# Performance work log

Hardware: AMD Instinct MI355X
Metric: run time of the kernel (lower is better)

The kernel has to match this reference:

```python
import jax, jax.numpy as jnp
import numpy as np

INNER = 256   # inner_channel
NODES = 64    # nodes_num (prototypes)
EM_NUM = 3
DIAG_C = 128  # hardcoded diag_channel in FullyConnectGCLayer


def setup_inputs() -> dict:
    key = jax.random.key(0)
    ks = jax.random.split(key, 16)
    b, c, w, h = 4, 1024, 64, 64
    f32 = jnp.float32
    d = {}
    d["x"] = jax.random.normal(ks[0], (b, c, w, h), f32)
    # Conv2d weights re-initialized to N(0, 0.001) in Intra_graph.__init__
    d["W_in"] = 0.001 * jax.random.normal(ks[1], (INNER, c), f32)
    d["b_in"] = jnp.zeros((INNER,), f32)
    d["multi_proto"] = 0.001 * jax.random.normal(ks[2], (1, INNER, NODES), f32)
    d["pi0"] = jnp.ones((1, NODES), f32) / NODES
    # Conv1d layers keep default kaiming-uniform-ish init
    lim = 1.0 / np.sqrt(INNER)
    d["W_adj"] = jax.random.uniform(ks[3], (DIAG_C, INNER), f32, -lim, lim)
    d["b_adj"] = jax.random.uniform(ks[4], (DIAG_C,), f32, -lim, lim)
    d["W_diag"] = jax.random.uniform(ks[5], (DIAG_C, INNER), f32, -lim, lim)
    d["b_diag"] = jax.random.uniform(ks[6], (DIAG_C,), f32, -lim, lim)
    d["gcn_weight"] = 0.01 * jax.random.normal(ks[7], (INNER, INNER), f32)
    d["W_out"] = 0.001 * jax.random.normal(ks[8], (c, INNER), f32)
    d["b_out"] = jnp.zeros((c,), f32)
    d["gamma"] = jnp.ones((c,), f32)
    d["beta"] = jnp.zeros((c,), f32)
    d["W_out2"] = 0.001 * jax.random.normal(ks[9], (c, INNER), f32)
    d["b_out2"] = jnp.zeros((c,), f32)
    d["gamma2"] = jnp.ones((c,), f32)
    d["beta2"] = jnp.zeros((c,), f32)
    d["flag"] = 0
    return d


def _bn(y, g, bt):
    # BatchNorm2d in training mode: batch stats over (N,H,W), biased var, eps=1e-5
    m = jnp.mean(y, (0, 2, 3), keepdims=True)
    v = jnp.var(y, (0, 2, 3), keepdims=True)
    return (y - m) * jax.lax.rsqrt(v + 1e-5) * g[None, :, None, None] + bt[None, :, None, None]


def _forward(x, W_in, b_in, multi_proto, pi0, W_adj, b_adj, W_diag, b_diag,
             gcn_weight, W_out, b_out, gamma, beta, W_out2, b_out2, gamma2, beta2):
    b, c, w, h = x.shape
    wh = w * h
    x1 = (jnp.einsum('oi,bihw->bohw', W_in, x) + b_in[None, :, None, None]).reshape(b, INNER, wh)
    # ---- EM soft-clustering loop (runs under no_grad in torch) ----
    x1s = jax.lax.stop_gradient(x1)
    mu = jnp.broadcast_to(multi_proto, (b, INNER, NODES))
    pi = jnp.broadcast_to(pi0[None, :, :], (b, 1, NODES))
    for _ in range(EM_NUM):
        lik = jnp.einsum('bcm,bcn->bmn', x1s, mu)              # [b, wh, n]
        lik = jnp.exp(lik - jnp.max(lik, 2, keepdims=True))
        post = lik * pi
        post = post / (1e-18 + jnp.sum(post, 2, keepdims=True))
        prob = post / (1e-18 + jnp.sum(post, 1, keepdims=True))
        mu = jnp.einsum('bcm,bmn->bcn', x1s, prob)
        pi = jnp.sum(post, 1, keepdims=True) / wh
    post = jax.lax.stop_gradient(post)
    prob = jax.lax.stop_gradient(prob)
    # ---- aggregate to prototypes (grad flows through x1 only) ----
    x2 = jnp.einsum('bcm,bmn->bcn', x1, prob)                   # [b, inner, n]
    # ---- branch 2: scatter back, conv, bn ----
    x4 = jnp.einsum('bcn,bmn->bcm', x2, post).reshape(b, INNER, w, h)
    x4 = _bn(jnp.einsum('oi,bihw->bohw', W_out2, x4) + b_out2[None, :, None, None], gamma2, beta2)
    output2 = jax.nn.relu(jax.nn.relu(x4) + x)
    # ---- FullyConnectGCLayer on x2 ----
    xd = jnp.einsum('oi,bin->bon', W_diag, x2) + b_diag[None, :, None]
    dvec = jax.nn.sigmoid(jnp.mean(xd, 2))                      # [b, 128]
    xa = jnp.einsum('oi,bin->bon', W_adj, x2) + b_adj[None, :, None]  # [b, 128, n]
    # sigmoid(diag(d)) has 0.5 off-diagonal, sigmoid(d) on diagonal:
    # xa^T S xa = 0.5 * (1^T xa)^T (1^T xa) + xa^T diag(sig(d)-0.5) xa
    u = jnp.sum(xa, 1)                                          # [b, n]
    A = 0.5 * u[:, :, None] * u[:, None, :] + jnp.einsum('bcn,bc,bcm->bnm', xa, dvec - 0.5, xa)
    A = jax.nn.relu(A) + jnp.eye(NODES, dtype=x.dtype)[None]
    deg = jax.lax.stop_gradient(jnp.sum(A, 1) ** -0.5)          # no_grad degree, [b, n]
    A = deg[:, :, None] * A * deg[:, None, :]
    gout = jnp.einsum('oi,bin->bon', gcn_weight, jnp.einsum('bcn,bnm->bcm', x2, A))
    x2g = jax.nn.relu(gout) + x2                                # res_connect
    # ---- branch 1: scatter back, conv, bn ----
    x3 = jnp.einsum('bcn,bmn->bcm', x2g, post).reshape(b, INNER, w, h)
    x3 = _bn(jnp.einsum('oi,bihw->bohw', W_out, x3) + b_out[None, :, None, None], gamma, beta)
    output = jax.nn.relu(jax.nn.relu(x3) + x)
    return output, output2


def reference(x, W_in, b_in, multi_proto, pi0, W_adj, b_adj, W_diag, b_diag,
              gcn_weight, W_out, b_out, gamma, beta, W_out2, b_out2, gamma2, beta2, flag):
    # flag only gates a buffer EMA update (no effect on forward outputs)
    return _forward(x, W_in, b_in, multi_proto, pi0, W_adj, b_adj, W_diag, b_diag,
                    gcn_weight, W_out, b_out, gamma, beta, W_out2, b_out2, gamma2, beta2)
```

## Files before the change

### kernel.cpp

```cpp
#include <hip/hip_runtime.h>
#include <math.h>


typedef unsigned short u16;
typedef short s16x8 __attribute__((ext_vector_type(8)));
typedef float f32x4 __attribute__((ext_vector_type(4)));

constexpr int BB  = 4;
constexpr int CH  = 1024;
constexpr int IN  = 256;
constexpr int ND  = 64;
constexpr int WH  = 4096;
constexpr int DCN = 128;
constexpr size_t TOT = (size_t)BB * CH * WH;

__device__ inline u16 f2bf(float f) {
  unsigned u = __float_as_uint(f);
  return (u16)((u + 0x7fffu + ((u >> 16) & 1u)) >> 16);
}
__device__ inline s16x8 ld8(const u16* p) { return *(const s16x8*)p; }
#define MFMA16(a, b, c) __builtin_amdgcn_mfma_f32_16x16x32_bf16(a, b, c, 0, 0, 0)

__global__ void k_init(const float* __restrict__ Win, const float* __restrict__ mp,
                       const float* __restrict__ pi0, u16* __restrict__ Winb,
                       u16* __restrict__ mu_t, float* __restrict__ piw,
                       float* __restrict__ sp) {
  int idx = blockIdx.x * 256 + threadIdx.x;
  if (idx < IN * CH) { Winb[idx] = f2bf(Win[idx]); return; }
  int j = idx - IN * CH;
  if (j < BB * ND * IN) {
    int bb = j >> 14, n = (j >> 8) & 63, c = j & 255;
    mu_t[((size_t)(bb * ND + n)) * IN + c] = f2bf(mp[c * ND + n]);
    return;
  }
  j -= BB * ND * IN;
  if (j < BB * ND) { piw[j] = pi0[j & 63]; return; }
  j -= BB * ND;
  if (j < 3 * BB * ND) sp[j] = 0.f;
}

__global__ __launch_bounds__(512) void k_x1(
    const float* __restrict__ x, const u16* __restrict__ Winb,
    const float* __restrict__ bin, u16* __restrict__ x1, u16* __restrict__ x1t) {
  __shared__ u16 lt[64][40];
  const int t = threadIdx.x, w = t >> 6, lr = t & 15, lg = (t >> 4) & 3;
  const int wc = w & 3, wm = w >> 2;
  const int m0 = blockIdx.x * 64, b = blockIdx.y;
  const int si = t >> 4, sm = (t & 15) * 4;
  const float* xb = x + (size_t)b * CH * WH + m0 + sm;
  f32x4 acc[4][2];
#pragma unroll
  for (int i = 0; i < 4; ++i)
#pragma unroll
    for (int j = 0; j < 2; ++j) acc[i][j] = (f32x4){0.f, 0.f, 0.f, 0.f};
  const u16* wp = Winb + (size_t)(wc * 64 + lr) * CH + lg * 8;

  float4 nxt = *(const float4*)&xb[(size_t)si * WH];
  for (int k0 = 0; k0 < CH; k0 += 32) {
    float4 cur = nxt;
    __syncthreads();
    lt[sm + 0][si] = f2bf(cur.x); lt[sm + 1][si] = f2bf(cur.y);
    lt[sm + 2][si] = f2bf(cur.z); lt[sm + 3][si] = f2bf(cur.w);
    if (k0 + 32 < CH) nxt = *(const float4*)&xb[(size_t)(k0 + 32 + si) * WH];
    __syncthreads();
    s16x8 af[4], bf[2];
#pragma unroll
    for (int i = 0; i < 4; ++i) af[i] = ld8(wp + (size_t)i * 16 * CH + k0);
#pragma unroll
    for (int j = 0; j < 2; ++j) bf[j] = *(const s16x8*)&lt[wm * 32 + j * 16 + lr][lg * 8];
#pragma unroll
    for (int i = 0; i < 4; ++i)
#pragma unroll
      for (int j = 0; j < 2; ++j) acc[i][j] = MFMA16(af[i], bf[j], acc[i][j]);
  }
#pragma unroll
  for (int i = 0; i < 4; ++i) {
    const int cb = wc * 64 + i * 16 + lg * 4;
    const float4 bi = *(const float4*)&bin[cb];
    const float bia[4] = {bi.x, bi.y, bi.z, bi.w};
#pragma unroll
    for (int j = 0; j < 2; ++j) {
      const int m = m0 + wm * 32 + j * 16 + lr;
      float v[4];
#pragma unroll
      for (int r = 0; r < 4; ++r) v[r] = acc[i][j][r] + bia[r];
      ushort4 o;
      o.x = f2bf(v[0]); o.y = f2bf(v[1]); o.z = f2bf(v[2]); o.w = f2bf(v[3]);
      *(ushort4*)&x1t[((size_t)b * WH + m) * IN + cb] = o;
#pragma unroll
      for (int r = 0; r < 4; ++r)
        x1[((size_t)b * IN + cb + r) * WH + m] = f2bf(v[r]);
    }
  }
}

__global__ __launch_bounds__(256) void k_em(
    const u16* __restrict__ x1, const u16* __restrict__ x1t,
    const u16* __restrict__ mu_t, const float* __restrict__ piw,
    float* __restrict__ sp, u16* __restrict__ pmn,
    float* __restrict__ mup, float* __restrict__ gp, int doLast) {
  __shared__ u16 ptl[64][264];
  const int t = threadIdx.x, w = t >> 6, lr = t & 15, lg = (t >> 4) & 3;
  const int mch = blockIdx.x, b = blockIdx.y;
  const int mbase = mch * 256;
  {
    f32x4 acc[4][4];
#pragma unroll
    for (int i = 0; i < 4; ++i)
#pragma unroll
      for (int f = 0; f < 4; ++f) acc[i][f] = (f32x4){0.f, 0.f, 0.f, 0.f};
    const u16* ap = x1t + ((size_t)b * WH + mbase + w * 64 + lr) * IN + lg * 8;
    const u16* bp = mu_t + ((size_t)b * ND + lr) * IN + lg * 8;
#pragma unroll
    for (int k0 = 0; k0 < IN; k0 += 32) {
      s16x8 bf[4];
#pragma unroll
      for (int f = 0; f < 4; ++f) bf[f] = ld8(bp + f * 16 * IN + k0);
#pragma unroll
      for (int i = 0; i < 4; ++i) {
        s16x8 av = ld8(ap + (size_t)i * 16 * IN + k0);
#pragma unroll
        for (int f = 0; f < 4; ++f) acc[i][f] = MFMA16(av, bf[f], acc[i][f]);
      }
    }
    float pi_[4], spart[4] = {0.f, 0.f, 0.f, 0.f};
#pragma unroll
    for (int f = 0; f < 4; ++f) pi_[f] = piw[b * ND + f * 16 + lr];
#pragma unroll
    for (int i = 0; i < 4; ++i)
#pragma unroll
      for (int r = 0; r < 4; ++r) {
        float v0 = acc[i][0][r], v1 = acc[i][1][r], v2 = acc[i][2][r], v3 = acc[i][3][r];
        float mx = fmaxf(fmaxf(v0, v1), fmaxf(v2, v3));
        mx = fmaxf(mx, __shfl_xor(mx, 1)); mx = fmaxf(mx, __shfl_xor(mx, 2));
        mx = fmaxf(mx, __shfl_xor(mx, 4)); mx = fmaxf(mx, __shfl_xor(mx, 8));
        float e0 = __expf(v0 - mx) * pi_[0], e1 = __expf(v1 - mx) * pi_[1];
        float e2 = __expf(v2 - mx) * pi_[2], e3 = __expf(v3 - mx) * pi_[3];
        float s = e0 + e1 + e2 + e3;
        s += __shfl_xor(s, 1); s += __shfl_xor(s, 2);
        s += __shfl_xor(s, 4); s += __shfl_xor(s, 8);
        const float inv = 1.f / (1e-18f + s);
        e0 *= inv; e1 *= inv; e2 *= inv; e3 *= inv;
        const int mloc = w * 64 + i * 16 + lg * 4 + r;
        u16 q0 = f2bf(e0), q1 = f2bf(e1), q2 = f2bf(e2), q3 = f2bf(e3);
        ptl[0 + lr][mloc]  = q0; ptl[16 + lr][mloc] = q1;
        ptl[32 + lr][mloc] = q2; ptl[48 + lr][mloc] = q3;
        if (doLast) {
          const size_t gbase = ((size_t)b * WH + mbase + mloc) * ND + lr;
          pmn[gbase + 0]  = q0; pmn[gbase + 16] = q1;
          pmn[gbase + 32] = q2; pmn[gbase + 48] = q3;
        }
        spart[0] += e0; spart[1] += e1; spart[2] += e2; spart[3] += e3;
      }
#pragma unroll
    for (int f = 0; f < 4; ++f) {
      spart[f] += __shfl_xor(spart[f], 16);
      spart[f] += __shfl_xor(spart[f], 32);
    }
    if (((t >> 4) & 3) == 0) {
#pragma unroll
      for (int f = 0; f < 4; ++f)
        atomicAdd(&sp[b * ND + f * 16 + lr], spart[f]);
    }
  }
  __syncthreads();
  {
    f32x4 acc[4][4];
#pragma unroll
    for (int i = 0; i < 4; ++i)
#pragma unroll
      for (int j = 0; j < 4; ++j) acc[i][j] = (f32x4){0.f, 0.f, 0.f, 0.f};
    const u16* ap = x1 + ((size_t)b * IN + w * 64 + lr) * WH + mbase + lg * 8;
#pragma unroll
    for (int ks = 0; ks < 8; ++ks) {
      s16x8 af[4], bf[4];
#pragma unroll
      for (int i = 0; i < 4; ++i) af[i] = ld8(ap + (size_t)i * 16 * WH + ks * 32);
#pragma unroll
      for (int j = 0; j < 4; ++j)
        bf[j] = *(const s16x8*)&ptl[j * 16 + lr][ks * 32 + lg * 8];
#pragma unroll
      for (int i = 0; i < 4; ++i)
#pragma unroll
        for (int j = 0; j < 4; ++j) acc[i][j] = MFMA16(af[i], bf[j], acc[i][j]);
    }
    float* mo = mup + ((size_t)mch * BB + b) * (IN * ND);
#pragma unroll
    for (int i = 0; i < 4; ++i)
#pragma unroll
      for (int j = 0; j < 4; ++j)
#pragma unroll
        for (int r = 0; r < 4; ++r) {
          const int c = w * 64 + i * 16 + lg * 4 + r, n = j * 16 + lr;
          mo[c * ND + n] = acc[i][j][r];
        }
  }
  if (doLast) {
    f32x4 acc[4];
#pragma unroll
    for (int j = 0; j < 4; ++j) acc[j] = (f32x4){0.f, 0.f, 0.f, 0.f};
#pragma unroll
    for (int ks = 0; ks < 8; ++ks) {
      s16x8 av = *(const s16x8*)&ptl[w * 16 + lr][ks * 32 + lg * 8];
#pragma unroll
      for (int j = 0; j < 4; ++j) {
        s16x8 bq = *(const s16x8*)&ptl[j * 16 + lr][ks * 32 + lg * 8];
        acc[j] = MFMA16(av, bq, acc[j]);
      }
    }
    float* go = gp + ((size_t)mch * BB + b) * (ND * ND);
#pragma unroll
    for (int j = 0; j < 4; ++j)
#pragma unroll
      for (int r = 0; r < 4; ++r) {
        const int n1 = w * 16 + lg * 4 + r, n2 = j * 16 + lr;
        go[n1 * ND + n2] = acc[j][r];
      }
  }
}

__global__ void k_mu_red(const float* __restrict__ mup, const float* __restrict__ spb,
                         float* __restrict__ piw, float* __restrict__ mu,
                         u16* __restrict__ mu_t, const float* __restrict__ gp,
                         float* __restrict__ G, int doG) {
  const int idx = blockIdx.x * 256 + threadIdx.x;
  const int bb = idx >> 14, c = (idx >> 6) & 255, n = idx & 63;
  float s = 0.f;
#pragma unroll
  for (int ch = 0; ch < 16; ++ch)
    s += mup[((size_t)ch * BB + bb) * (IN * ND) + (idx & 16383)];
  const float v = s / (1e-18f + spb[bb * ND + n]);
  mu[idx] = v;
  mu_t[((size_t)(bb * ND + n)) * IN + c] = f2bf(v);
  if (idx < BB * ND) piw[idx] = spb[idx] * (1.f / (float)WH);
  if (doG && idx < BB * ND * ND) {
    float g = 0.f;
#pragma unroll
    for (int ch = 0; ch < 16; ++ch) g += gp[(size_t)ch * (BB * ND * ND) + idx];
    G[idx] = g;
  }
}

__device__ void zg_body(const float* __restrict__ W, const float* __restrict__ v,
                        float* __restrict__ z, u16* __restrict__ zb,
                        int o0, int bb, int t, char* smem) {
  float (*As)[68] = (float(*)[68])smem;
  float (*Bs)[64] = (float(*)[64])(smem + 4352);
  const int tx = t & 15, ty = t >> 4;
  const int aoo = t >> 2, akq = (t & 3) * 4;
  const int bkk = t >> 4, bnq = (t & 15) * 4;
  float acc[4][4] = {};
  for (int k0 = 0; k0 < IN; k0 += 16) {
    {
      float4 w4 = *(const float4*)&W[(size_t)(o0 + aoo) * IN + k0 + akq];
      As[akq + 0][aoo] = w4.x; As[akq + 1][aoo] = w4.y;
      As[akq + 2][aoo] = w4.z; As[akq + 3][aoo] = w4.w;
    }
    *(float4*)&Bs[bkk][bnq] = *(const float4*)&v[((size_t)bb * IN + k0 + bkk) * ND + bnq];
    __syncthreads();
#pragma unroll
    for (int kk = 0; kk < 16; ++kk) {
      float4 a4 = *(const float4*)&As[kk][ty * 4];
      float4 b4 = *(const float4*)&Bs[kk][tx * 4];
      float ar[4] = {a4.x, a4.y, a4.z, a4.w}, br[4] = {b4.x, b4.y, b4.z, b4.w};
#pragma unroll
      for (int i = 0; i < 4; ++i)
#pragma unroll
        for (int j = 0; j < 4; ++j) acc[i][j] += ar[i] * br[j];
    }
    __syncthreads();
  }
#pragma unroll
  for (int i = 0; i < 4; ++i) {
    float4 r = make_float4(acc[i][0], acc[i][1], acc[i][2], acc[i][3]);
    const size_t off = ((size_t)bb * CH + o0 + ty * 4 + i) * ND + tx * 4;
    *(float4*)&z[off] = r;
    ushort4 h;
    h.x = f2bf(r.x); h.y = f2bf(r.y); h.z = f2bf(r.z); h.w = f2bf(r.w);
    *(ushort4*)&zb[off] = h;
  }
}

__global__ __launch_bounds__(256) void k_gcAz2(
    const float* __restrict__ mu, const float* __restrict__ gw,
    const float* __restrict__ Wa, const float* __restrict__ ba,
    const float* __restrict__ Wd, const float* __restrict__ bd,
    float* __restrict__ qbuf, float* __restrict__ xabuf, float* __restrict__ dv,
    const float* __restrict__ Wo2, float* __restrict__ z2, u16* __restrict__ zb2) {
  __shared__ __align__(16) char smem[66560];
  const int t = threadIdx.x, bid = blockIdx.x;
  if (bid < 28) {
    const int blk = bid % 7, b = bid / 7;
    float* sx2 = (float*)smem;
    float* srm = (float*)(smem + 65536);
    if (blk < 6) {
      const float* src = mu + (size_t)b * IN * ND;
#pragma unroll
      for (int q4 = 0; q4 < 16; ++q4)
        *(float4*)&sx2[q4 * 1024 + t * 4] = *(const float4*)&src[q4 * 1024 + t * 4];
      __syncthreads();
      const int rg = t >> 4, cg2 = t & 15;
      const float* W = (blk < 4) ? gw + (size_t)(blk * 64 + rg * 4) * IN
                                 : Wa + (size_t)((blk - 4) * 64 + rg * 4) * IN;
      float acc[4][4] = {};
      for (int i4 = 0; i4 < 64; ++i4) {
        float4 xv[4];
#pragma unroll
        for (int e = 0; e < 4; ++e)
          xv[e] = *(const float4*)&sx2[(i4 * 4 + e) * 64 + cg2 * 4];
#pragma unroll
        for (int rr = 0; rr < 4; ++rr) {
          const float4 w4 = *(const float4*)&W[(size_t)rr * IN + i4 * 4];
          acc[rr][0] += w4.x * xv[0].x + w4.y * xv[1].x + w4.z * xv[2].x + w4.w * xv[3].x;
          acc[rr][1] += w4.x * xv[0].y + w4.y * xv[1].y + w4.z * xv[2].y + w4.w * xv[3].y;
          acc[rr][2] += w4.x * xv[0].z + w4.y * xv[1].z + w4.z * xv[2].z + w4.w * xv[3].z;
          acc[rr][3] += w4.x * xv[0].w + w4.y * xv[1].w + w4.z * xv[2].w + w4.w * xv[3].w;
        }
      }
      if (blk < 4) {
        float* dst = qbuf + (size_t)b * IN * ND + (size_t)(blk * 64 + rg * 4) * ND + cg2 * 4;
#pragma unroll
        for (int rr = 0; rr < 4; ++rr)
          *(float4*)&dst[(size_t)rr * ND] =
              make_float4(acc[rr][0], acc[rr][1], acc[rr][2], acc[rr][3]);
      } else {
        const int xr = (blk - 4) * 64 + rg * 4;
        float* dst = xabuf + (size_t)b * DCN * ND + (size_t)xr * ND + cg2 * 4;
#pragma unroll
        for (int rr = 0; rr < 4; ++rr) {
          const float bv = ba[xr + rr];
          *(float4*)&dst[(size_t)rr * ND] =
              make_float4(acc[rr][0] + bv, acc[rr][1] + bv, acc[rr][2] + bv, acc[rr][3] + bv);
        }
      }
    } else {
      {
        const float* row = mu + (size_t)b * IN * ND + (size_t)t * ND;
        float s = 0.f;
#pragma unroll
        for (int n4 = 0; n4 < 16; ++n4) {
          float4 v = *(const float4*)&row[n4 * 4];
          s += v.x + v.y + v.z + v.w;
        }
        srm[t] = s * (1.f / ND);
      }
      __syncthreads();
      if (t < DCN) {
        float av = 0.f;
#pragma unroll
        for (int i4 = 0; i4 < 64; ++i4) {
          float4 w4 = *(const float4*)&Wd[(size_t)t * IN + i4 * 4];
          float4 r4 = *(const float4*)&srm[i4 * 4];
          av += w4.x * r4.x + w4.y * r4.y + w4.z * r4.z + w4.w * r4.w;
        }
        av += bd[t];
        dv[b * DCN + t] = 1.f / (1.f + __expf(-av)) - 0.5f;
      }
    }
  } else if (bid >= 32 && bid < 96) {
    const int zid = bid - 32;
    zg_body(Wo2, mu, z2, zb2, (zid & 15) * 64, zid >> 4, t, smem);
  }
}

__global__ __launch_bounds__(256) void k_gcBC(
    const float* __restrict__ xabuf, const float* __restrict__ dv,
    const float* __restrict__ qbuf, const float* __restrict__ mu,
    float* __restrict__ x2g) {
  __shared__ float sxa[DCN * ND];
  __shared__ float sA[ND * 65];
  __shared__ float sq[64 * 68];
  __shared__ float sdv[DCN];
  __shared__ float su[ND];
  __shared__ float sdeg[ND];
  const int t = threadIdx.x, qtr = blockIdx.x, b = blockIdx.y;
  {
    const float* src = xabuf + (size_t)b * DCN * ND;
#pragma unroll
    for (int q4 = 0; q4 < 8; ++q4)
      *(float4*)&sxa[q4 * 1024 + t * 4] = *(const float4*)&src[q4 * 1024 + t * 4];
    if (t < DCN) sdv[t] = dv[b * DCN + t];
    const int r = t >> 2, seg = (t & 3) * 16;
    const float* qs = qbuf + (size_t)b * IN * ND + (size_t)(qtr * 64 + r) * ND + seg;
#pragma unroll
    for (int f = 0; f < 4; ++f) {
      float4 v = *(const float4*)&qs[f * 4];
      sq[r * 68 + seg + f * 4 + 0] = v.x; sq[r * 68 + seg + f * 4 + 1] = v.y;
      sq[r * 68 + seg + f * 4 + 2] = v.z; sq[r * 68 + seg + f * 4 + 3] = v.w;
    }
  }
  __syncthreads();
  if (t < ND) {
    float s = 0.f;
    for (int dc = 0; dc < DCN; ++dc) s += sxa[dc * ND + t];
    su[t] = s;
  }
  __syncthreads();
  {
    const int n1g = t >> 4, n2g = t & 15;
    float acc[4][4] = {};
    for (int dc = 0; dc < DCN; ++dc) {
      const float dvv = sdv[dc];
      float4 v1 = *(const float4*)&sxa[dc * ND + n1g * 4];
      const float4 v2 = *(const float4*)&sxa[dc * ND + n2g * 4];
      v1.x *= dvv; v1.y *= dvv; v1.z *= dvv; v1.w *= dvv;
      acc[0][0] += v1.x * v2.x; acc[0][1] += v1.x * v2.y;
      acc[0][2] += v1.x * v2.z; acc[0][3] += v1.x * v2.w;
      acc[1][0] += v1.y * v2.x; acc[1][1] += v1.y * v2.y;
      acc[1][2] += v1.y * v2.z; acc[1][3] += v1.y * v2.w;
      acc[2][0] += v1.z * v2.x; acc[2][1] += v1.z * v2.y;
      acc[2][2] += v1.z * v2.z; acc[2][3] += v1.z * v2.w;
      acc[3][0] += v1.w * v2.x; acc[3][1] += v1.w * v2.y;
      acc[3][2] += v1.w * v2.z; acc[3][3] += v1.w * v2.w;
    }
#pragma unroll
    for (int i = 0; i < 4; ++i) {
      const int n1 = n1g * 4 + i;
      const float u1 = su[n1];
#pragma unroll
      for (int j = 0; j < 4; ++j) {
        const int n2 = n2g * 4 + j;
        const float v = acc[i][j] + 0.5f * u1 * su[n2];
        sA[n1 * 65 + n2] = fmaxf(v, 0.f) + (n1 == n2 ? 1.f : 0.f);
      }
    }
  }
  __syncthreads();
  if (t < ND) {
    float s = 0.f;
    for (int m = 0; m < ND; ++m) s += sA[m * 65 + t];
    sdeg[t] = rsqrtf(s);
  }
  __syncthreads();
  {
    const int n1g = t >> 4, n2g = t & 15;
#pragma unroll
    for (int i = 0; i < 4; ++i) {
      const int n1 = n1g * 4 + i;
      const float dr = sdeg[n1];
#pragma unroll
      for (int e = 0; e < 4; ++e)
        sA[n1 * 65 + n2g * 4 + e] *= dr * sdeg[n2g * 4 + e];
    }
  }
  __syncthreads();
  {
    const int rg = t >> 4, cg2 = t & 15;
    float acc[4][4] = {};
    for (int k = 0; k < ND; ++k) {
      const float4 a4 = *(const float4*)&sA[k * 65 + cg2 * 4];
      float qv[4];
#pragma unroll
      for (int rr = 0; rr < 4; ++rr) qv[rr] = sq[(rg * 4 + rr) * 68 + k];
#pragma unroll
      for (int rr = 0; rr < 4; ++rr) {
        acc[rr][0] += qv[rr] * a4.x; acc[rr][1] += qv[rr] * a4.y;
        acc[rr][2] += qv[rr] * a4.z; acc[rr][3] += qv[rr] * a4.w;
      }
    }
#pragma unroll
    for (int rr = 0; rr < 4; ++rr) {
      const size_t off = (size_t)b * IN * ND + (size_t)(qtr * 64 + rg * 4 + rr) * ND + cg2 * 4;
      const float4 xv = *(const float4*)&mu[off];
      float4 o;
      o.x = fmaxf(acc[rr][0], 0.f) + xv.x; o.y = fmaxf(acc[rr][1], 0.f) + xv.y;
      o.z = fmaxf(acc[rr][2], 0.f) + xv.z; o.w = fmaxf(acc[rr][3], 0.f) + xv.w;
      *(float4*)&x2g[off] = o;
    }
  }
}

__global__ __launch_bounds__(256) void k_zg(
    const float* __restrict__ W, const float* __restrict__ v,
    float* __restrict__ z, u16* __restrict__ zb) {
  __shared__ __align__(16) char smem[8448];
  zg_body(W, v, z, zb, blockIdx.x * 64, blockIdx.y, threadIdx.x, smem);
}

__global__ __launch_bounds__(256) void k_stats(
    const float* __restrict__ z1, const float* __restrict__ z2,
    const float* __restrict__ sp, const float* __restrict__ G,
    const float* __restrict__ gam, const float* __restrict__ bet,
    const float* __restrict__ gam2, const float* __restrict__ bet2,
    float* __restrict__ abc) {
  const int t = threadIdx.x;
  const int o = blockIdx.x * 4 + (t >> 6), lane = t & 63;
#pragma unroll
  for (int br = 0; br < 2; ++br) {
    const float* z = br ? z2 : z1;
    float macc = 0.f, eacc = 0.f;
    for (int bb = 0; bb < BB; ++bb) {
      const float zv = z[((size_t)bb * CH + o) * ND + lane];
      float s1 = zv * sp[bb * ND + lane];
      const float* Gb = G + (size_t)bb * ND * ND;
      float gz = 0.f;
      for (int k = 0; k < ND; ++k) {
        const float zk = __shfl(zv, k);
        gz += Gb[k * ND + lane] * zk;
      }
      float q = zv * gz;
#pragma unroll
      for (int off = 32; off; off >>= 1) {
        s1 += __shfl_xor(s1, off);
        q  += __shfl_xor(q, off);
      }
      macc += s1; eacc += q;
    }
    const float inv = 1.f / (float)((size_t)BB * WH);
    const float mean = macc * inv;
    const float var  = eacc * inv - mean * mean;
    const float a = (br ? gam2[o] : gam[o]) * rsqrtf(var + 1e-5f);
    const float c = (br ? bet2[o] : bet[o]) - mean * a;
    if (lane == 0) { abc[br * 2 * CH + o] = a; abc[br * 2 * CH + CH + o] = c; }
  }
}

__global__ __launch_bounds__(256) void k_epi(
    const u16* __restrict__ zb1, const u16* __restrict__ zb2,
    const u16* __restrict__ post, const float* __restrict__ abc,
    const float* __restrict__ x, float* __restrict__ out1, float* __restrict__ out2) {
  const int t = threadIdx.x, w = t >> 6, lr = t & 15, lg = (t >> 4) & 3;
  const int m0 = blockIdx.x * 256 + w * 64, o0 = blockIdx.y * 64, bb = blockIdx.z;
  f32x4 acc1[4][4], acc2[4][4];
#pragma unroll
  for (int i = 0; i < 4; ++i)
#pragma unroll
    for (int j = 0; j < 4; ++j) {
      acc1[i][j] = (f32x4){0.f, 0.f, 0.f, 0.f};
      acc2[i][j] = (f32x4){0.f, 0.f, 0.f, 0.f};
    }
  const u16* z1p = zb1 + ((size_t)bb * CH + o0 + lr) * ND + lg * 8;
  const u16* z2p = zb2 + ((size_t)bb * CH + o0 + lr) * ND + lg * 8;
  const u16* pp  = post + ((size_t)bb * WH + m0 + lr) * ND + lg * 8;
#pragma unroll
  for (int ks = 0; ks < 2; ++ks) {
    s16x8 a1[4], a2[4], bq[4];
#pragma unroll
    for (int i = 0; i < 4; ++i) {
      a1[i] = ld8(z1p + i * 16 * ND + ks * 32);
      a2[i] = ld8(z2p + i * 16 * ND + ks * 32);
    }
#pragma unroll
    for (int j = 0; j < 4; ++j) bq[j] = ld8(pp + j * 16 * ND + ks * 32);
#pragma unroll
    for (int i = 0; i < 4; ++i)
#pragma unroll
      for (int j = 0; j < 4; ++j) {
        acc1[i][j] = MFMA16(a1[i], bq[j], acc1[i][j]);
        acc2[i][j] = MFMA16(a2[i], bq[j], acc2[i][j]);
      }
  }
#pragma unroll
  for (int i = 0; i < 4; ++i)
#pragma unroll
    for (int r = 0; r < 4; ++r) {
      const int o = o0 + i * 16 + lg * 4 + r;
      const float a1v = abc[o], c1v = abc[CH + o];
      const float a2v = abc[2 * CH + o], c2v = abc[3 * CH + o];
      const size_t base = ((size_t)bb * CH + o) * WH + m0 + lr;
#pragma unroll
      for (int j = 0; j < 4; ++j) {
        const size_t off = base + j * 16;
        const float xv = __builtin_nontemporal_load(&x[off]);
        const float r1 = fmaxf(fmaxf(a1v * acc1[i][j][r] + c1v, 0.f) + xv, 0.f);
        const float r2 = fmaxf(fmaxf(a2v * acc2[i][j][r] + c2v, 0.f) + xv, 0.f);
        __builtin_nontemporal_store(r1, &out1[off]);
        __builtin_nontemporal_store(r2, &out2[off]);
      }
    }
}

extern "C" void kernel_launch(void* const* d_in, const int* in_sizes, int n_in,
                              void* d_out, int out_size, void* d_ws, size_t ws_size,
                              hipStream_t stream) {
  (void)in_sizes; (void)n_in; (void)out_size; (void)ws_size;
  const float* x    = (const float*)d_in[0];
  const float* Win  = (const float*)d_in[1];
  const float* bin  = (const float*)d_in[2];
  const float* mp   = (const float*)d_in[3];
  const float* pi0  = (const float*)d_in[4];
  const float* Wa   = (const float*)d_in[5];
  const float* ba   = (const float*)d_in[6];
  const float* Wd   = (const float*)d_in[7];
  const float* bd   = (const float*)d_in[8];
  const float* gw   = (const float*)d_in[9];
  const float* Wo   = (const float*)d_in[10];
  const float* gam  = (const float*)d_in[12];
  const float* bet  = (const float*)d_in[13];
  const float* Wo2  = (const float*)d_in[14];
  const float* gam2 = (const float*)d_in[16];
  const float* bet2 = (const float*)d_in[17];

  char* ob = (char*)d_out;
  char* wp = (char*)d_ws;
  float* mup = (float*)(ob + 0);
  float* gp  = (float*)(ob + 4194304);
  float* z1  = (float*)(ob + 5242880);
  float* z2  = (float*)(ob + 6291456);
  u16*   x1    = (u16*)(wp + 0);
  u16*   x1t   = (u16*)(wp + 8388608);
  u16*   Winb  = (u16*)(wp + 16777216);
  u16*   mu_t  = (u16*)(wp + 17301504);
  u16*   pmn   = (u16*)(wp + 17432576);
  float* mu    = (float*)(wp + 19529728);
  float* x2g   = (float*)(wp + 19791872);
  u16*   zb1   = (u16*)(wp + 20054016);
  u16*   zb2   = (u16*)(wp + 20578304);
  float* sp3   = (float*)(wp + 21102592);
  float* piw   = (float*)(wp + 21105664);
  float* abc   = (float*)(wp + 21106688);
  float* G     = (float*)(wp + 21123072);
  float* qbuf  = (float*)(wp + 21188608);
  float* xabuf = (float*)(wp + 21450752);
  float* dvb   = (float*)(wp + 21581824);
  float* out1  = (float*)d_out;
  float* out2  = out1 + TOT;

  k_init<<<dim3(1284), 256, 0, stream>>>(Win, mp, pi0, Winb, mu_t, piw, sp3);
  k_x1<<<dim3(64, BB), 512, 0, stream>>>(x, Winb, bin, x1, x1t);
  for (int it = 0; it < 3; ++it) {
    float* spb = sp3 + it * 256;
    const int doLast = (it == 2);
    k_em<<<dim3(16, BB), 256, 0, stream>>>(x1, x1t, mu_t, piw, spb, pmn, mup, gp, doLast);
    k_mu_red<<<dim3(256), 256, 0, stream>>>(mup, spb, piw, mu, mu_t, gp, G, doLast);
  }
  k_gcAz2<<<dim3(96), 256, 0, stream>>>(mu, gw, Wa, ba, Wd, bd, qbuf, xabuf, dvb,
                                        Wo2, z2, zb2);
  k_gcBC<<<dim3(4, BB), 256, 0, stream>>>(xabuf, dvb, qbuf, mu, x2g);
  k_zg<<<dim3(16, BB), 256, 0, stream>>>(Wo, x2g, z1, zb1);
  k_stats<<<dim3(256), 256, 0, stream>>>(z1, z2, sp3 + 512, G, gam, bet, gam2, bet2, abc);
  k_epi<<<dim3(16, 16, BB), 256, 0, stream>>>(zb1, zb2, pmn, abc, x, out1, out2);
}
```

Before: 276.5 us.

## Split EM into more blocks with bf16 partials; fuse BN stats into zg

The EM kernel grid grows from 16 to 64 spatial chunks per batch, with each block handling 64 positions instead of 256, so more CUs are busy. Per-chunk mu and G partials are now stored as bf16 to limit the extra reduction traffic, and k_mu_red sums 64 partials instead of 16. The separate k_stats kernel is removed: BatchNorm mean and variance terms are computed inside the zg GEMM body and accumulated with atomics, and the scale and shift are finished in k_epi. The trade-off is lower precision in the mu partial sums and more atomic traffic.

```diff
diff --git a/kernel.cpp b/kernel.cpp
--- a/kernel.cpp
+++ b/kernel.cpp
@@ -18,13 +18,14 @@
   unsigned u = __float_as_uint(f);
   return (u16)((u + 0x7fffu + ((u >> 16) & 1u)) >> 16);
 }
+__device__ inline float bf2f(u16 u) { return __uint_as_float((unsigned)u << 16); }
 __device__ inline s16x8 ld8(const u16* p) { return *(const s16x8*)p; }
 #define MFMA16(a, b, c) __builtin_amdgcn_mfma_f32_16x16x32_bf16(a, b, c, 0, 0, 0)
 
 __global__ void k_init(const float* __restrict__ Win, const float* __restrict__ mp,
                        const float* __restrict__ pi0, u16* __restrict__ Winb,
                        u16* __restrict__ mu_t, float* __restrict__ piw,
-                       float* __restrict__ sp) {
+                       float* __restrict__ sp3, float* __restrict__ sbuf) {
   int idx = blockIdx.x * 256 + threadIdx.x;
   if (idx < IN * CH) { Winb[idx] = f2bf(Win[idx]); return; }
   int j = idx - IN * CH;
@@ -36,7 +37,9 @@
   j -= BB * ND * IN;
   if (j < BB * ND) { piw[j] = pi0[j & 63]; return; }
   j -= BB * ND;
-  if (j < 3 * BB * ND) sp[j] = 0.f;
+  if (j < 3 * BB * ND) { sp3[j] = 0.f; return; }
+  j -= 3 * BB * ND;
+  if (j < 4 * CH) sbuf[j] = 0.f;
 }
 
 __global__ __launch_bounds__(512) void k_x1(
@@ -98,60 +101,50 @@
     const u16* __restrict__ x1, const u16* __restrict__ x1t,
     const u16* __restrict__ mu_t, const float* __restrict__ piw,
     float* __restrict__ sp, u16* __restrict__ pmn,
-    float* __restrict__ mup, float* __restrict__ gp, int doLast) {
-  __shared__ u16 ptl[64][264];
+    u16* __restrict__ mup16, u16* __restrict__ gp16, int doLast) {
+  __shared__ u16 ptl[64][72];
   const int t = threadIdx.x, w = t >> 6, lr = t & 15, lg = (t >> 4) & 3;
   const int mch = blockIdx.x, b = blockIdx.y;
-  const int mbase = mch * 256;
   {
-    f32x4 acc[4][4];
-#pragma unroll
-    for (int i = 0; i < 4; ++i)
-#pragma unroll
-      for (int f = 0; f < 4; ++f) acc[i][f] = (f32x4){0.f, 0.f, 0.f, 0.f};
-    const u16* ap = x1t + ((size_t)b * WH + mbase + w * 64 + lr) * IN + lg * 8;
+    f32x4 acc[4];
+#pragma unroll
+    for (int f = 0; f < 4; ++f) acc[f] = (f32x4){0.f, 0.f, 0.f, 0.f};
+    const u16* ap = x1t + ((size_t)b * WH + mch * 64 + w * 16 + lr) * IN + lg * 8;
     const u16* bp = mu_t + ((size_t)b * ND + lr) * IN + lg * 8;
 #pragma unroll
     for (int k0 = 0; k0 < IN; k0 += 32) {
-      s16x8 bf[4];
-#pragma unroll
-      for (int f = 0; f < 4; ++f) bf[f] = ld8(bp + f * 16 * IN + k0);
-#pragma unroll
-      for (int i = 0; i < 4; ++i) {
-        s16x8 av = ld8(ap + (size_t)i * 16 * IN + k0);
-#pragma unroll
-        for (int f = 0; f < 4; ++f) acc[i][f] = MFMA16(av, bf[f], acc[i][f]);
-      }
+      s16x8 av = ld8(ap + k0);
+#pragma unroll
+      for (int f = 0; f < 4; ++f)
+        acc[f] = MFMA16(av, ld8(bp + f * 16 * IN + k0), acc[f]);
     }
     float pi_[4], spart[4] = {0.f, 0.f, 0.f, 0.f};
 #pragma unroll
     for (int f = 0; f < 4; ++f) pi_[f] = piw[b * ND + f * 16 + lr];
 #pragma unroll
-    for (int i = 0; i < 4; ++i)
-#pragma unroll
-      for (int r = 0; r < 4; ++r) {
-        float v0 = acc[i][0][r], v1 = acc[i][1][r], v2 = acc[i][2][r], v3 = acc[i][3][r];
-        float mx = fmaxf(fmaxf(v0, v1), fmaxf(v2, v3));
-        mx = fmaxf(mx, __shfl_xor(mx, 1)); mx = fmaxf(mx, __shfl_xor(mx, 2));
-        mx = fmaxf(mx, __shfl_xor(mx, 4)); mx = fmaxf(mx, __shfl_xor(mx, 8));
-        float e0 = __expf(v0 - mx) * pi_[0], e1 = __expf(v1 - mx) * pi_[1];
-        float e2 = __expf(v2 - mx) * pi_[2], e3 = __expf(v3 - mx) * pi_[3];
-        float s = e0 + e1 + e2 + e3;
-        s += __shfl_xor(s, 1); s += __shfl_xor(s, 2);
-        s += __shfl_xor(s, 4); s += __shfl_xor(s, 8);
-        const float inv = 1.f / (1e-18f + s);
-        e0 *= inv; e1 *= inv; e2 *= inv; e3 *= inv;
-        const int mloc = w * 64 + i * 16 + lg * 4 + r;
-        u16 q0 = f2bf(e0), q1 = f2bf(e1), q2 = f2bf(e2), q3 = f2bf(e3);
-        ptl[0 + lr][mloc]  = q0; ptl[16 + lr][mloc] = q1;
-        ptl[32 + lr][mloc] = q2; ptl[48 + lr][mloc] = q3;
-        if (doLast) {
-          const size_t gbase = ((size_t)b * WH + mbase + mloc) * ND + lr;
-          pmn[gbase + 0]  = q0; pmn[gbase + 16] = q1;
-          pmn[gbase + 32] = q2; pmn[gbase + 48] = q3;
-        }
-        spart[0] += e0; spart[1] += e1; spart[2] += e2; spart[3] += e3;
-      }
+    for (int r = 0; r < 4; ++r) {
+      float v0 = acc[0][r], v1 = acc[1][r], v2 = acc[2][r], v3 = acc[3][r];
+      float mx = fmaxf(fmaxf(v0, v1), fmaxf(v2, v3));
+      mx = fmaxf(mx, __shfl_xor(mx, 1)); mx = fmaxf(mx, __shfl_xor(mx, 2));
+      mx = fmaxf(mx, __shfl_xor(mx, 4)); mx = fmaxf(mx, __shfl_xor(mx, 8));
+      float e0 = __expf(v0 - mx) * pi_[0], e1 = __expf(v1 - mx) * pi_[1];
+      float e2 = __expf(v2 - mx) * pi_[2], e3 = __expf(v3 - mx) * pi_[3];
+      float s = e0 + e1 + e2 + e3;
+      s += __shfl_xor(s, 1); s += __shfl_xor(s, 2);
+      s += __shfl_xor(s, 4); s += __shfl_xor(s, 8);
+      const float inv = 1.f / (1e-18f + s);
+      e0 *= inv; e1 *= inv; e2 *= inv; e3 *= inv;
+      const int mloc = w * 16 + lg * 4 + r;
+      u16 q0 = f2bf(e0), q1 = f2bf(e1), q2 = f2bf(e2), q3 = f2bf(e3);
+      ptl[0 + lr][mloc]  = q0; ptl[16 + lr][mloc] = q1;
+      ptl[32 + lr][mloc] = q2; ptl[48 + lr][mloc] = q3;
+      if (doLast) {
+        const size_t gbase = ((size_t)b * WH + mch * 64 + mloc) * ND + lr;
+        pmn[gbase + 0]  = q0; pmn[gbase + 16] = q1;
+        pmn[gbase + 32] = q2; pmn[gbase + 48] = q3;
+      }
+      spart[0] += e0; spart[1] += e1; spart[2] += e2; spart[3] += e3;
+    }
 #pragma unroll
     for (int f = 0; f < 4; ++f) {
       spart[f] += __shfl_xor(spart[f], 16);
@@ -170,9 +163,9 @@
     for (int i = 0; i < 4; ++i)
 #pragma unroll
       for (int j = 0; j < 4; ++j) acc[i][j] = (f32x4){0.f, 0.f, 0.f, 0.f};
-    const u16* ap = x1 + ((size_t)b * IN + w * 64 + lr) * WH + mbase + lg * 8;
-#pragma unroll
-    for (int ks = 0; ks < 8; ++ks) {
+    const u16* ap = x1 + ((size_t)b * IN + w * 64 + lr) * WH + mch * 64 + lg * 8;
+#pragma unroll
+    for (int ks = 0; ks < 2; ++ks) {
       s16x8 af[4], bf[4];
 #pragma unroll
       for (int i = 0; i < 4; ++i) af[i] = ld8(ap + (size_t)i * 16 * WH + ks * 32);
@@ -184,7 +177,7 @@
 #pragma unroll
         for (int j = 0; j < 4; ++j) acc[i][j] = MFMA16(af[i], bf[j], acc[i][j]);
     }
-    float* mo = mup + ((size_t)mch * BB + b) * (IN * ND);
+    u16* mo = mup16 + ((size_t)mch * BB + b) * (IN * ND);
 #pragma unroll
     for (int i = 0; i < 4; ++i)
 #pragma unroll
@@ -192,7 +185,7 @@
 #pragma unroll
         for (int r = 0; r < 4; ++r) {
           const int c = w * 64 + i * 16 + lg * 4 + r, n = j * 16 + lr;
-          mo[c * ND + n] = acc[i][j][r];
+          mo[c * ND + n] = f2bf(acc[i][j][r]);
         }
   }
   if (doLast) {
@@ -200,7 +193,7 @@
 #pragma unroll
     for (int j = 0; j < 4; ++j) acc[j] = (f32x4){0.f, 0.f, 0.f, 0.f};
 #pragma unroll
-    for (int ks = 0; ks < 8; ++ks) {
+    for (int ks = 0; ks < 2; ++ks) {
       s16x8 av = *(const s16x8*)&ptl[w * 16 + lr][ks * 32 + lg * 8];
 #pragma unroll
       for (int j = 0; j < 4; ++j) {
@@ -208,44 +201,48 @@
         acc[j] = MFMA16(av, bq, acc[j]);
       }
     }
-    float* go = gp + ((size_t)mch * BB + b) * (ND * ND);
+    u16* go = gp16 + ((size_t)mch * BB + b) * (ND * ND);
 #pragma unroll
     for (int j = 0; j < 4; ++j)
 #pragma unroll
       for (int r = 0; r < 4; ++r) {
         const int n1 = w * 16 + lg * 4 + r, n2 = j * 16 + lr;
-        go[n1 * ND + n2] = acc[j][r];
-      }
-  }
-}
-
-__global__ void k_mu_red(const float* __restrict__ mup, const float* __restrict__ spb,
+        go[n1 * ND + n2] = f2bf(acc[j][r]);
+      }
+  }
+}
+
+__global__ void k_mu_red(const u16* __restrict__ mup16, const float* __restrict__ spb,
                          float* __restrict__ piw, float* __restrict__ mu,
-                         u16* __restrict__ mu_t, const float* __restrict__ gp,
+                         u16* __restrict__ mu_t, const u16* __restrict__ gp16,
                          float* __restrict__ G, int doG) {
   const int idx = blockIdx.x * 256 + threadIdx.x;
   const int bb = idx >> 14, c = (idx >> 6) & 255, n = idx & 63;
   float s = 0.f;
-#pragma unroll
-  for (int ch = 0; ch < 16; ++ch)
-    s += mup[((size_t)ch * BB + bb) * (IN * ND) + (idx & 16383)];
+#pragma unroll 8
+  for (int ch = 0; ch < 64; ++ch)
+    s += bf2f(mup16[((size_t)ch * BB + bb) * (IN * ND) + (idx & 16383)]);
   const float v = s / (1e-18f + spb[bb * ND + n]);
   mu[idx] = v;
   mu_t[((size_t)(bb * ND + n)) * IN + c] = f2bf(v);
   if (idx < BB * ND) piw[idx] = spb[idx] * (1.f / (float)WH);
   if (doG && idx < BB * ND * ND) {
     float g = 0.f;
-#pragma unroll
-    for (int ch = 0; ch < 16; ++ch) g += gp[(size_t)ch * (BB * ND * ND) + idx];
+#pragma unroll 8
+    for (int ch = 0; ch < 64; ++ch)
+      g += bf2f(gp16[(size_t)ch * (BB * ND * ND) + idx]);
     G[idx] = g;
   }
 }
 
-__device__ void zg_body(const float* __restrict__ W, const float* __restrict__ v,
-                        float* __restrict__ z, u16* __restrict__ zb,
-                        int o0, int bb, int t, char* smem) {
+__device__ void zg_stats_body(const float* __restrict__ W, const float* __restrict__ v,
+                              u16* __restrict__ zb, int o0, int bb, int t, char* smem,
+                              const float* __restrict__ sp, const float* __restrict__ G,
+                              float* __restrict__ sbm, float* __restrict__ sbe) {
   float (*As)[68] = (float(*)[68])smem;
   float (*Bs)[64] = (float(*)[64])(smem + 4352);
+  float (*sz)[68] = (float(*)[68])(smem + 8448);
+  float* sG = (float*)(smem + 8448 + 17408);
   const int tx = t & 15, ty = t >> 4;
   const int aoo = t >> 2, akq = (t & 3) * 4;
   const int bkk = t >> 4, bnq = (t & 15) * 4;
@@ -272,12 +269,42 @@
   }
 #pragma unroll
   for (int i = 0; i < 4; ++i) {
-    float4 r = make_float4(acc[i][0], acc[i][1], acc[i][2], acc[i][3]);
     const size_t off = ((size_t)bb * CH + o0 + ty * 4 + i) * ND + tx * 4;
-    *(float4*)&z[off] = r;
     ushort4 h;
-    h.x = f2bf(r.x); h.y = f2bf(r.y); h.z = f2bf(r.z); h.w = f2bf(r.w);
+    h.x = f2bf(acc[i][0]); h.y = f2bf(acc[i][1]);
+    h.z = f2bf(acc[i][2]); h.w = f2bf(acc[i][3]);
     *(ushort4*)&zb[off] = h;
+#pragma unroll
+    for (int j = 0; j < 4; ++j) sz[ty * 4 + i][tx * 4 + j] = acc[i][j];
+  }
+  {
+    const float* Gb = G + (size_t)bb * ND * ND;
+#pragma unroll
+    for (int q = 0; q < 4; ++q)
+      *(float4*)&sG[q * 1024 + t * 4] = *(const float4*)&Gb[q * 1024 + t * 4];
+  }
+  __syncthreads();
+  float spv[4];
+#pragma unroll
+  for (int j = 0; j < 4; ++j) spv[j] = sp[bb * ND + tx * 4 + j];
+#pragma unroll
+  for (int i = 0; i < 4; ++i) {
+    float s1 = acc[i][0] * spv[0] + acc[i][1] * spv[1] +
+               acc[i][2] * spv[2] + acc[i][3] * spv[3];
+    float q = 0.f;
+    const float* zrow = sz[ty * 4 + i];
+    for (int k = 0; k < ND; ++k) {
+      const float zk = zrow[k];
+      const float4 g4 = *(const float4*)&sG[k * 64 + tx * 4];
+      q += zk * (g4.x * acc[i][0] + g4.y * acc[i][1] +
+                 g4.z * acc[i][2] + g4.w * acc[i][3]);
+    }
+#pragma unroll
+    for (int o = 1; o <= 8; o <<= 1) { s1 += __shfl_xor(s1, o); q += __shfl_xor(q, o); }
+    if ((t & 15) == 0) {
+      atomicAdd(&sbm[o0 + ty * 4 + i], s1);
+      atomicAdd(&sbe[o0 + ty * 4 + i], q);
+    }
   }
 }
 
@@ -286,7 +313,9 @@
     const float* __restrict__ Wa, const float* __restrict__ ba,
     const float* __restrict__ Wd, const float* __restrict__ bd,
     float* __restrict__ qbuf, float* __restrict__ xabuf, float* __restrict__ dv,
-    const float* __restrict__ Wo2, float* __restrict__ z2, u16* __restrict__ zb2) {
+    const float* __restrict__ Wo2, u16* __restrict__ zb2,
+    const float* __restrict__ spL, const float* __restrict__ G,
+    float* __restrict__ sbuf) {
   __shared__ __align__(16) char smem[66560];
   const int t = threadIdx.x, bid = blockIdx.x;
   if (bid < 28) {
@@ -359,7 +388,8 @@
     }
   } else if (bid >= 32 && bid < 96) {
     const int zid = bid - 32;
-    zg_body(Wo2, mu, z2, zb2, (zid & 15) * 64, zid >> 4, t, smem);
+    zg_stats_body(Wo2, mu, zb2, (zid & 15) * 64, zid >> 4, t, smem,
+                  spL, G, sbuf + 2 * CH, sbuf + 3 * CH);
   }
 }
 
@@ -471,56 +501,32 @@
 }
 
 __global__ __launch_bounds__(256) void k_zg(
-    const float* __restrict__ W, const float* __restrict__ v,
-    float* __restrict__ z, u16* __restrict__ zb) {
-  __shared__ __align__(16) char smem[8448];
-  zg_body(W, v, z, zb, blockIdx.x * 64, blockIdx.y, threadIdx.x, smem);
-}
-
-__global__ __launch_bounds__(256) void k_stats(
-    const float* __restrict__ z1, const float* __restrict__ z2,
-    const float* __restrict__ sp, const float* __restrict__ G,
+    const float* __restrict__ W, const float* __restrict__ v, u16* __restrict__ zb,
+    const float* __restrict__ spL, const float* __restrict__ G,
+    float* __restrict__ sbuf) {
+  __shared__ __align__(16) char smem[42240];
+  zg_stats_body(W, v, zb, blockIdx.x * 64, blockIdx.y, threadIdx.x, smem,
+                spL, G, sbuf, sbuf + CH);
+}
+
+__global__ __launch_bounds__(256) void k_epi(
+    const u16* __restrict__ zb1, const u16* __restrict__ zb2,
+    const u16* __restrict__ post, const float* __restrict__ sbuf,
     const float* __restrict__ gam, const float* __restrict__ bet,
     const float* __restrict__ gam2, const float* __restrict__ bet2,
-    float* __restrict__ abc) {
-  const int t = threadIdx.x;
-  const int o = blockIdx.x * 4 + (t >> 6), lane = t & 63;
-#pragma unroll
-  for (int br = 0; br < 2; ++br) {
-    const float* z = br ? z2 : z1;
-    float macc = 0.f, eacc = 0.f;
-    for (int bb = 0; bb < BB; ++bb) {
-      const float zv = z[((size_t)bb * CH + o) * ND + lane];
-      float s1 = zv * sp[bb * ND + lane];
-      const float* Gb = G + (size_t)bb * ND * ND;
-      float gz = 0.f;
-      for (int k = 0; k < ND; ++k) {
-        const float zk = __shfl(zv, k);
-        gz += Gb[k * ND + lane] * zk;
-      }
-      float q = zv * gz;
-#pragma unroll
-      for (int off = 32; off; off >>= 1) {
-        s1 += __shfl_xor(s1, off);
-        q  += __shfl_xor(q, off);
-      }
-      macc += s1; eacc += q;
-    }
+    const float* __restrict__ x, float* __restrict__ out1, float* __restrict__ out2) {
+  __shared__ float sabc[4][64];
+  const int t = threadIdx.x, w = t >> 6, lr = t & 15, lg = (t >> 4) & 3;
+  const int m0 = blockIdx.x * 256 + w * 64, o0 = blockIdx.y * 64, bb = blockIdx.z;
+  if (t < 128) {
+    const int br = t >> 6, oo = t & 63, o = o0 + oo;
     const float inv = 1.f / (float)((size_t)BB * WH);
-    const float mean = macc * inv;
-    const float var  = eacc * inv - mean * mean;
+    const float mean = sbuf[br * 2 * CH + o] * inv;
+    const float var  = sbuf[(br * 2 + 1) * CH + o] * inv - mean * mean;
     const float a = (br ? gam2[o] : gam[o]) * rsqrtf(var + 1e-5f);
     const float c = (br ? bet2[o] : bet[o]) - mean * a;
-    if (lane == 0) { abc[br * 2 * CH + o] = a; abc[br * 2 * CH + CH + o] = c; }
-  }
-}
-
-__global__ __launch_bounds__(256) void k_epi(
-    const u16* __restrict__ zb1, const u16* __restrict__ zb2,
-    const u16* __restrict__ post, const float* __restrict__ abc,
-    const float* __restrict__ x, float* __restrict__ out1, float* __restrict__ out2) {
-  const int t = threadIdx.x, w = t >> 6, lr = t & 15, lg = (t >> 4) & 3;
-  const int m0 = blockIdx.x * 256 + w * 64, o0 = blockIdx.y * 64, bb = blockIdx.z;
+    sabc[br * 2][oo] = a; sabc[br * 2 + 1][oo] = c;
+  }
   f32x4 acc1[4][4], acc2[4][4];
 #pragma unroll
   for (int i = 0; i < 4; ++i)
@@ -550,14 +556,15 @@
         acc2[i][j] = MFMA16(a2[i], bq[j], acc2[i][j]);
       }
   }
+  __syncthreads();
 #pragma unroll
   for (int i = 0; i < 4; ++i)
 #pragma unroll
     for (int r = 0; r < 4; ++r) {
-      const int o = o0 + i * 16 + lg * 4 + r;
-      const float a1v = abc[o], c1v = abc[CH + o];
-      const float a2v = abc[2 * CH + o], c2v = abc[3 * CH + o];
-      const size_t base = ((size_t)bb * CH + o) * WH + m0 + lr;
+      const int oo = i * 16 + lg * 4 + r;
+      const float a1v = sabc[0][oo], c1v = sabc[1][oo];
+      const float a2v = sabc[2][oo], c2v = sabc[3][oo];
+      const size_t base = ((size_t)bb * CH + o0 + oo) * WH + m0 + lr;
 #pragma unroll
       for (int j = 0; j < 4; ++j) {
         const size_t off = base + j * 16;
@@ -593,10 +600,8 @@
 
   char* ob = (char*)d_out;
   char* wp = (char*)d_ws;
-  float* mup = (float*)(ob + 0);
-  float* gp  = (float*)(ob + 4194304);
-  float* z1  = (float*)(ob + 5242880);
-  float* z2  = (float*)(ob + 6291456);
+  u16* mup16 = (u16*)(ob + 0);
+  u16* gp16  = (u16*)(ob + 8388608);
   u16*   x1    = (u16*)(wp + 0);
   u16*   x1t   = (u16*)(wp + 8388608);
   u16*   Winb  = (u16*)(wp + 16777216);
@@ -608,26 +613,29 @@
   u16*   zb2   = (u16*)(wp + 20578304);
   float* sp3   = (float*)(wp + 21102592);
   float* piw   = (float*)(wp + 21105664);
-  float* abc   = (float*)(wp + 21106688);
-  float* G     = (float*)(wp + 21123072);
-  float* qbuf  = (float*)(wp + 21188608);
-  float* xabuf = (float*)(wp + 21450752);
-  float* dvb   = (float*)(wp + 21581824);
+  float* G     = (float*)(wp + 21106688);
+  float* qbuf  = (float*)(wp + 21172224);
+  float* xabuf = (float*)(wp + 21434368);
+  float* dvb   = (float*)(wp + 21565440);
+  float* sbuf  = (float*)(wp + 21567488);
   float* out1  = (float*)d_out;
   float* out2  = out1 + TOT;
-
-  k_init<<<dim3(1284), 256, 0, stream>>>(Win, mp, pi0, Winb, mu_t, piw, sp3);
+  float* spL   = sp3 + 512;
+
+  k_init<<<dim3(1317), 256, 0, stream>>>(Win, mp, pi0, Winb, mu_t, piw, sp3, sbuf);
   k_x1<<<dim3(64, BB), 512, 0, stream>>>(x, Winb, bin, x1, x1t);
   for (int it = 0; it < 3; ++it) {
     float* spb = sp3 + it * 256;
     const int doLast = (it == 2);
-    k_em<<<dim3(16, BB), 256, 0, stream>>>(x1, x1t, mu_t, piw, spb, pmn, mup, gp, doLast);
-    k_mu_red<<<dim3(256), 256, 0, stream>>>(mup, spb, piw, mu, mu_t, gp, G, doLast);
+    k_em<<<dim3(64, BB), 256, 0, stream>>>(x1, x1t, mu_t, piw, spb, pmn,
+                                           mup16, gp16, doLast);
+    k_mu_red<<<dim3(256), 256, 0, stream>>>(mup16, spb, piw, mu, mu_t,
+                                            gp16, G, doLast);
   }
   k_gcAz2<<<dim3(96), 256, 0, stream>>>(mu, gw, Wa, ba, Wd, bd, qbuf, xabuf, dvb,
-                                        Wo2, z2, zb2);
+                                        Wo2, zb2, spL, G, sbuf);
   k_gcBC<<<dim3(4, BB), 256, 0, stream>>>(xabuf, dvb, qbuf, mu, x2g);
-  k_zg<<<dim3(16, BB), 256, 0, stream>>>(Wo, x2g, z1, zb1);
-  k_stats<<<dim3(256), 256, 0, stream>>>(z1, z2, sp3 + 512, G, gam, bet, gam2, bet2, abc);
-  k_epi<<<dim3(16, 16, BB), 256, 0, stream>>>(zb1, zb2, pmn, abc, x, out1, out2);
-}
+  k_zg<<<dim3(16, BB), 256, 0, stream>>>(Wo, x2g, zb1, spL, G, sbuf);
+  k_epi<<<dim3(16, 16, BB), 256, 0, stream>>>(zb1, zb2, pmn, sbuf,
+                                              gam, bet, gam2, bet2, x, out1, out2);
+}
```

New measurement: 251.6 us. 1.1x faster.
